# Performance work log

Hardware: AMD Instinct MI355X
Metric: run time of the kernel (lower is better)

Reference implementation:

```python
import jax, jax.numpy as jnp
import numpy as np
from jax import lax

CHANS = [3, 4, 8, 16, 32, 64, 128]


def _conv_relu(x, w, b):
    # x: [B,Cin,H,W], w: [Cout,Cin,4,4], stride 2, pad 1
    y = lax.conv_general_dilated(x, w, (2, 2), [(1, 1), (1, 1)],
                                 dimension_numbers=('NCHW', 'OIHW', 'NCHW'))
    return jax.nn.relu(y + b[None, :, None, None])


def setup_inputs() -> dict:
    key = jax.random.key(0)
    ks = jax.random.split(key, 64)
    T, B, S = 3, 2048, 64
    d = {"img_seq": jax.random.normal(ks[0], (T, B, 3, S, S), jnp.float32)}
    i = 1
    for l in range(6):
        cin, cout = CHANS[l], CHANS[l + 1]
        d[f"enc_w{l}"] = jax.random.normal(ks[i], (T, cout, cin, 4, 4), jnp.float32) / np.sqrt(cin * 16); i += 1
        d[f"enc_b{l}"] = jnp.zeros((T, cout), jnp.float32)
    # MLP 128 -> 32 -> 32 -> 64
    d["mlp_w1"] = jax.random.normal(ks[i], (32, 128), jnp.float32) / np.sqrt(128.0); i += 1
    d["mlp_b1"] = jnp.zeros((32,), jnp.float32)
    d["mlp_w2"] = jax.random.normal(ks[i], (32, 32), jnp.float32) / np.sqrt(32.0); i += 1
    d["mlp_b2"] = jnp.zeros((32,), jnp.float32)
    d["mlp_w3"] = jax.random.normal(ks[i], (64, 32), jnp.float32) / np.sqrt(32.0); i += 1
    d["mlp_b3"] = jnp.zeros((64,), jnp.float32)
    # LSTM: input 64, hidden 20 (torch gate order i,f,g,o)
    H = 20
    d["w_ih"] = jax.random.normal(ks[i], (4 * H, 64), jnp.float32) / np.sqrt(64.0); i += 1
    d["w_hh"] = jax.random.normal(ks[i], (4 * H, H), jnp.float32) / np.sqrt(float(H)); i += 1
    d["b_ih"] = jnp.zeros((4 * H,), jnp.float32)
    d["b_hh"] = jnp.zeros((4 * H,), jnp.float32)
    # 20 reward heads: 20 -> 32 -> 32 -> 1, stacked on leading K axis
    K = 20
    d["head_w1"] = jax.random.normal(ks[i], (K, 32, H), jnp.float32) / np.sqrt(float(H)); i += 1
    d["head_b1"] = jnp.zeros((K, 32), jnp.float32)
    d["head_w2"] = jax.random.normal(ks[i], (K, 32, 32), jnp.float32) / np.sqrt(32.0); i += 1
    d["head_b2"] = jnp.zeros((K, 32), jnp.float32)
    d["head_w3"] = jax.random.normal(ks[i], (K, 1, 32), jnp.float32) / np.sqrt(32.0); i += 1
    d["head_b3"] = jnp.zeros((K, 1), jnp.float32)
    return d


def reference(img_seq,
              enc_w0, enc_b0, enc_w1, enc_b1, enc_w2, enc_b2,
              enc_w3, enc_b3, enc_w4, enc_b4, enc_w5, enc_b5,
              mlp_w1, mlp_b1, mlp_w2, mlp_b2, mlp_w3, mlp_b3,
              w_ih, w_hh, b_ih, b_hh,
              head_w1, head_b1, head_w2, head_b2, head_w3, head_b3):
    # Per-frame CNN encoders (one encoder per time step) -> vmap over T
    def encode(img, w0, b0, w1, b1, w2, b2, w3, b3, w4, b4, w5, b5):
        x = _conv_relu(img, w0, b0)
        x = _conv_relu(x, w1, b1)
        x = _conv_relu(x, w2, b2)
        x = _conv_relu(x, w3, b3)
        x = _conv_relu(x, w4, b4)
        x = _conv_relu(x, w5, b5)  # [B,128,1,1]
        return x.reshape(x.shape[0], -1)  # [B,128]

    enc = jax.vmap(encode)(img_seq, enc_w0, enc_b0, enc_w1, enc_b1, enc_w2, enc_b2,
                           enc_w3, enc_b3, enc_w4, enc_b4, enc_w5, enc_b5)  # [T,B,128]

    # Shared MLP 128 -> 64
    h = jax.nn.relu(jnp.einsum('tbd,od->tbo', enc, mlp_w1) + mlp_b1)
    h = jax.nn.relu(jnp.einsum('tbd,od->tbo', h, mlp_w2) + mlp_b2)
    feats = jnp.einsum('tbd,od->tbo', h, mlp_w3) + mlp_b3  # [T,B,64]

    # Single-layer LSTM over T
    B, H = feats.shape[1], w_hh.shape[1]
    def step(carry, x_t):
        hs, cs = carry
        gates = x_t @ w_ih.T + hs @ w_hh.T + b_ih + b_hh  # [B,4H]
        i, f, g, o = jnp.split(gates, 4, axis=-1)
        cs = jax.nn.sigmoid(f) * cs + jax.nn.sigmoid(i) * jnp.tanh(g)
        hs = jax.nn.sigmoid(o) * jnp.tanh(cs)
        return (hs, cs), hs
    init = (jnp.zeros((B, H), feats.dtype), jnp.zeros((B, H), feats.dtype))
    _, h_seq = lax.scan(step, init, feats)  # [T,B,20]

    # 20 reward heads applied to every LSTM output, batched over head axis k
    x1 = jax.nn.relu(jnp.einsum('tbd,kod->ktbo', h_seq, head_w1) + head_b1[:, None, None, :])
    x2 = jax.nn.relu(jnp.einsum('ktbd,kod->ktbo', x1, head_w2) + head_b2[:, None, None, :])
    out = jnp.einsum('ktbd,kod->ktbo', x2, head_w3) + head_b3[:, None, None, :]  # [20,T,B,1]
    return out
```

## Files before the change

### kernel.cpp

```cpp
#include <hip/hip_runtime.h>
#include <math.h>

#define T_DIM 3
#define B_DIM 2048
#define NIMG  (T_DIM * B_DIM)


__global__ __launch_bounds__(256) void conv0_kernel(
    const float* __restrict__ img, const float* __restrict__ w0,
    const float* __restrict__ b0, float* __restrict__ a0)
{
    const int wid  = blockIdx.x * 4 + (threadIdx.x >> 6);
    const int lane = threadIdx.x & 63;
    const int half = wid & 1;
    const int oh   = (wid >> 1) & 31;
    const int g    = (wid >> 6) & 31;
    const int t    = wid >> 11;
    const int im   = g * 64 + lane;
    const size_t ib = ((size_t)t * 2048 + im) * 12288;
    const int ow0  = half * 16;

    float acc[4][16];
#pragma unroll
    for (int j = 0; j < 4; j++) {
        const float bv = b0[t * 4 + j];
#pragma unroll
        for (int k = 0; k < 16; k++) acc[j][k] = bv;
    }
    const float* wt = w0 + t * 192;

    for (int ci = 0; ci < 3; ci++) {
#pragma unroll
        for (int kh = 0; kh < 4; kh++) {
            const int ih = 2 * oh - 1 + kh;
            if ((unsigned)ih >= 64u) continue;
            const float* rp = img + ib + (size_t)(ci * 64 + ih) * 64 + 2 * ow0;
            float tap[34];
#pragma unroll
            for (int q = 0; q < 8; q++)
                *(float4*)&tap[1 + 4 * q] = *(const float4*)(rp + 4 * q);
            tap[0]  = (half == 0) ? 0.f : rp[-1];
            tap[33] = (half == 0) ? rp[32] : 0.f;
            float w_[4][4];
#pragma unroll
            for (int j = 0; j < 4; j++)
#pragma unroll
                for (int kw = 0; kw < 4; kw++)
                    w_[j][kw] = wt[((j * 3 + ci) * 4 + kh) * 4 + kw];
#pragma unroll
            for (int jj = 0; jj < 16; jj++)
#pragma unroll
                for (int kw = 0; kw < 4; kw++) {
                    const float x = tap[2 * jj + kw];
#pragma unroll
                    for (int j = 0; j < 4; j++)
                        acc[j][jj] = fmaf(x, w_[j][kw], acc[j][jj]);
                }
        }
    }
    const size_t ob0 = ((size_t)(t * 4096 + oh * 32 + ow0)) * 2048 + im;
#pragma unroll
    for (int j = 0; j < 4; j++)
#pragma unroll
        for (int k = 0; k < 16; k++)
            a0[ob0 + ((size_t)j * 1024 + k) * 2048] = fmaxf(acc[j][k], 0.f);
}

template<int CIN, int COUT, int IH, int OH, int CB>
__device__ __forceinline__ void convmid(
    const float* __restrict__ in, const float* __restrict__ gw,
    const float* __restrict__ gb, float* __restrict__ out,
    int t, int cg, int oh, int im)
{
    const int co0 = cg * CB;
    float acc[CB][OH];
#pragma unroll
    for (int j = 0; j < CB; j++) {
        const float bv = gb[t * COUT + co0 + j];
#pragma unroll
        for (int k = 0; k < OH; k++) acc[j][k] = bv;
    }
    const float* wt = gw + ((size_t)t * COUT + co0) * CIN * 16;
    const size_t inb = ((size_t)t * CIN) * (IH * IH) * 2048 + im;

#pragma unroll 4
    for (int ci = 0; ci < CIN; ci++) {
#pragma unroll
        for (int kh = 0; kh < 4; kh++) {
            const int ih = 2 * oh - 1 + kh;
            if ((unsigned)ih >= (unsigned)IH) continue;
            const float* rp = in + inb + (size_t)(ci * IH + ih) * IH * 2048;
            float tap[IH + 2];
            tap[0] = 0.f; tap[IH + 1] = 0.f;
#pragma unroll
            for (int iw = 0; iw < IH; iw++) tap[iw + 1] = rp[(size_t)iw * 2048];
            float w_[CB][4];
#pragma unroll
            for (int j = 0; j < CB; j++)
#pragma unroll
                for (int kw = 0; kw < 4; kw++)
                    w_[j][kw] = wt[((size_t)j * CIN + ci) * 16 + kh * 4 + kw];
#pragma unroll
            for (int ow = 0; ow < OH; ow++)
#pragma unroll
                for (int kw = 0; kw < 4; kw++) {
                    const float x = tap[2 * ow + kw];
#pragma unroll
                    for (int j = 0; j < CB; j++)
                        acc[j][ow] = fmaf(x, w_[j][kw], acc[j][ow]);
                }
        }
    }
    const size_t ob = ((size_t)(t * COUT + co0) * OH * OH + (size_t)oh * OH) * 2048 + im;
#pragma unroll
    for (int j = 0; j < CB; j++)
#pragma unroll
        for (int k = 0; k < OH; k++)
            out[ob + ((size_t)j * OH * OH + k) * 2048] = fmaxf(acc[j][k], 0.f);
}

__global__ __launch_bounds__(256) void conv1_kernel(
    const float* __restrict__ a0, const float* __restrict__ w,
    const float* __restrict__ b, float* __restrict__ a1)
{
    const int wid = blockIdx.x * 4 + (threadIdx.x >> 6);
    const int lane = threadIdx.x & 63;
    const int oh = wid & 15, cg = (wid >> 4) & 1, g = (wid >> 5) & 31, t = wid >> 10;
    convmid<4, 8, 32, 16, 4>(a0, w, b, a1, t, cg, oh, g * 64 + lane);
}

__global__ __launch_bounds__(256) void conv2_kernel(
    const float* __restrict__ a1, const float* __restrict__ w,
    const float* __restrict__ b, float* __restrict__ a2)
{
    const int wid = blockIdx.x * 4 + (threadIdx.x >> 6);
    const int lane = threadIdx.x & 63;
    const int oh = wid & 7, cg = (wid >> 3) & 3, g = (wid >> 5) & 31, t = wid >> 10;
    convmid<8, 16, 16, 8, 4>(a1, w, b, a2, t, cg, oh, g * 64 + lane);
}

__global__ __launch_bounds__(256) void conv3_kernel(
    const float* __restrict__ a2, const float* __restrict__ w,
    const float* __restrict__ b, float* __restrict__ a3)
{
    const int wid = blockIdx.x * 4 + (threadIdx.x >> 6);
    const int lane = threadIdx.x & 63;
    const int oh = wid & 3, cg = (wid >> 2) & 3, g = (wid >> 4) & 31, t = wid >> 9;
    convmid<16, 32, 8, 4, 8>(a2, w, b, a3, t, cg, oh, g * 64 + lane);
}

__global__ __launch_bounds__(256) void conv4_kernel(
    const float* __restrict__ a3, const float* __restrict__ w4,
    const float* __restrict__ b4, float* __restrict__ a4)
{
    const int wid = blockIdx.x * 4 + (threadIdx.x >> 6);
    const int lane = threadIdx.x & 63;
    const int cg = wid & 7, g = (wid >> 3) & 31, t = wid >> 8;
    const int im = g * 64 + lane;
    const int co0 = cg * 8;

    float acc[8][4];
#pragma unroll
    for (int j = 0; j < 8; j++) {
        const float bv = b4[t * 64 + co0 + j];
#pragma unroll
        for (int p = 0; p < 4; p++) acc[j][p] = bv;
    }
    const float* wt = w4 + ((size_t)t * 64 + co0) * 32 * 16;
    const size_t inb = ((size_t)t * 32) * 16 * 2048 + im;

    for (int ci = 0; ci < 32; ci++) {
        float tin[16];
#pragma unroll
        for (int p = 0; p < 16; p++)
            tin[p] = a3[inb + ((size_t)ci * 16 + p) * 2048];
#pragma unroll
        for (int kh = 0; kh < 4; kh++)
#pragma unroll
            for (int oh = 0; oh < 2; oh++) {
                const int ih = 2 * oh - 1 + kh;
                if (ih < 0 || ih > 3) continue;
#pragma unroll
                for (int ow = 0; ow < 2; ow++)
#pragma unroll
                    for (int kw = 0; kw < 4; kw++) {
                        const int iw = 2 * ow - 1 + kw;
                        if (iw < 0 || iw > 3) continue;
                        const float x = tin[ih * 4 + iw];
#pragma unroll
                        for (int j = 0; j < 8; j++)
                            acc[j][oh * 2 + ow] = fmaf(
                                x, wt[((size_t)j * 32 + ci) * 16 + kh * 4 + kw],
                                acc[j][oh * 2 + ow]);
                    }
            }
    }
#pragma unroll
    for (int j = 0; j < 8; j++)
#pragma unroll
        for (int p = 0; p < 4; p++)
            a4[(((size_t)t * 64 + co0 + j) * 4 + p) * 2048 + im] =
                fmaxf(acc[j][p], 0.f);
}

__global__ __launch_bounds__(256) void conv5_kernel(
    const float* __restrict__ a4, const float* __restrict__ w5,
    const float* __restrict__ b5, float* __restrict__ feats)
{
    const int wid = blockIdx.x * 4 + (threadIdx.x >> 6);
    const int lane = threadIdx.x & 63;
    const int cg = wid & 15, g = (wid >> 4) & 31, t = wid >> 9;
    const int im = g * 64 + lane;
    const int co0 = cg * 8;

    float acc[8];
#pragma unroll
    for (int j = 0; j < 8; j++) acc[j] = b5[t * 128 + co0 + j];
    const float* wt = w5 + ((size_t)t * 128 + co0) * 64 * 16;
    const size_t inb = ((size_t)t * 64) * 4 * 2048 + im;

#pragma unroll 4
    for (int ci = 0; ci < 64; ci++) {
        const float x0 = a4[inb + ((size_t)ci * 4 + 0) * 2048];
        const float x1 = a4[inb + ((size_t)ci * 4 + 1) * 2048];
        const float x2 = a4[inb + ((size_t)ci * 4 + 2) * 2048];
        const float x3 = a4[inb + ((size_t)ci * 4 + 3) * 2048];
#pragma unroll
        for (int j = 0; j < 8; j++) {
            const size_t wb = ((size_t)j * 64 + ci) * 16;
            acc[j] = fmaf(x0, wt[wb + 5],  acc[j]);
            acc[j] = fmaf(x1, wt[wb + 6],  acc[j]);
            acc[j] = fmaf(x2, wt[wb + 9],  acc[j]);
            acc[j] = fmaf(x3, wt[wb + 10], acc[j]);
        }
    }
#pragma unroll
    for (int j = 0; j < 8; j++)
        feats[((size_t)t * 128 + co0 + j) * 2048 + im] = fmaxf(acc[j], 0.f);
}

__device__ __forceinline__ float sigmoidf_(float x) { return 1.f / (1.f + expf(-x)); }

__global__ __launch_bounds__(64) void head_kernel(
    const float* __restrict__ feats,
    const float* __restrict__ mw1, const float* __restrict__ mb1,
    const float* __restrict__ mw2, const float* __restrict__ mb2,
    const float* __restrict__ mw3, const float* __restrict__ mb3,
    const float* __restrict__ wih, const float* __restrict__ whh,
    const float* __restrict__ bih, const float* __restrict__ bhh,
    const float* __restrict__ hw1, const float* __restrict__ hb1,
    const float* __restrict__ hw2, const float* __restrict__ hb2,
    const float* __restrict__ hw3, const float* __restrict__ hb3,
    float* __restrict__ out)
{
    const int b   = blockIdx.x;
    const int tid = threadIdx.x;
    __shared__ float sX[384];
    __shared__ float sH1[96];
    __shared__ float sH2[96];
    __shared__ float sF[192];
    __shared__ float sGates[80];
    __shared__ float sHs[20], sCs[20], sHseq[60];
    __shared__ float sA1[3 * 640];
    __shared__ float sA2[3 * 640];

    for (int i = tid; i < 384; i += 64)
        sX[i] = feats[(size_t)i * 2048 + b];
    __syncthreads();

    if (tid < 32) {
        const float4* wr = (const float4*)(mw1 + tid * 128);
        float a0 = mb1[tid], a1 = a0, a2 = a0;
        for (int d4 = 0; d4 < 32; d4++) {
            float4 w  = wr[d4];
            float4 x0 = ((const float4*)sX)[d4];
            float4 x1 = ((const float4*)sX)[32 + d4];
            float4 x2 = ((const float4*)sX)[64 + d4];
            a0 = fmaf(w.x, x0.x, a0); a0 = fmaf(w.y, x0.y, a0);
            a0 = fmaf(w.z, x0.z, a0); a0 = fmaf(w.w, x0.w, a0);
            a1 = fmaf(w.x, x1.x, a1); a1 = fmaf(w.y, x1.y, a1);
            a1 = fmaf(w.z, x1.z, a1); a1 = fmaf(w.w, x1.w, a1);
            a2 = fmaf(w.x, x2.x, a2); a2 = fmaf(w.y, x2.y, a2);
            a2 = fmaf(w.z, x2.z, a2); a2 = fmaf(w.w, x2.w, a2);
        }
        sH1[tid] = fmaxf(a0, 0.f); sH1[32 + tid] = fmaxf(a1, 0.f); sH1[64 + tid] = fmaxf(a2, 0.f);
    }
    __syncthreads();

    if (tid < 32) {
        const float* wr = mw2 + tid * 32;
        float a0 = mb2[tid], a1 = a0, a2 = a0;
#pragma unroll
        for (int d = 0; d < 32; d++) {
            float w = wr[d];
            a0 = fmaf(w, sH1[d], a0);
            a1 = fmaf(w, sH1[32 + d], a1);
            a2 = fmaf(w, sH1[64 + d], a2);
        }
        sH2[tid] = fmaxf(a0, 0.f); sH2[32 + tid] = fmaxf(a1, 0.f); sH2[64 + tid] = fmaxf(a2, 0.f);
    }
    __syncthreads();

    {
        const float* wr = mw3 + tid * 32;
        float a0 = mb3[tid], a1 = a0, a2 = a0;
#pragma unroll
        for (int d = 0; d < 32; d++) {
            float w = wr[d];
            a0 = fmaf(w, sH2[d], a0);
            a1 = fmaf(w, sH2[32 + d], a1);
            a2 = fmaf(w, sH2[64 + d], a2);
        }
        sF[tid] = a0; sF[64 + tid] = a1; sF[128 + tid] = a2;
    }
    if (tid < 20) { sHs[tid] = 0.f; sCs[tid] = 0.f; }
    __syncthreads();

    for (int t = 0; t < 3; t++) {
        for (int i = tid; i < 80; i += 64) {
            float a = bih[i] + bhh[i];
            const float4* wi = (const float4*)(wih + i * 64);
            const float4* xr = (const float4*)(sF + t * 64);
#pragma unroll
            for (int d4 = 0; d4 < 16; d4++) {
                float4 w = wi[d4]; float4 x = xr[d4];
                a = fmaf(w.x, x.x, a); a = fmaf(w.y, x.y, a);
                a = fmaf(w.z, x.z, a); a = fmaf(w.w, x.w, a);
            }
            const float* wh = whh + i * 20;
#pragma unroll
            for (int d = 0; d < 20; d++) a = fmaf(wh[d], sHs[d], a);
            sGates[i] = a;
        }
        __syncthreads();
        if (tid < 20) {
            float ig = sigmoidf_(sGates[tid]);
            float fg = sigmoidf_(sGates[20 + tid]);
            float g  = tanhf(sGates[40 + tid]);
            float og = sigmoidf_(sGates[60 + tid]);
            float c  = fg * sCs[tid] + ig * g;
            sCs[tid] = c;
            float h = og * tanhf(c);
            sHs[tid] = h;
            sHseq[t * 20 + tid] = h;
        }
        __syncthreads();
    }

    for (int i = tid; i < 640; i += 64) {
        float wrow[20];
        const float4* wr = (const float4*)(hw1 + i * 20);
#pragma unroll
        for (int q = 0; q < 5; q++) {
            float4 w = wr[q];
            wrow[q * 4 + 0] = w.x; wrow[q * 4 + 1] = w.y;
            wrow[q * 4 + 2] = w.z; wrow[q * 4 + 3] = w.w;
        }
        float bv = hb1[i];
        float a0 = bv, a1 = bv, a2 = bv;
#pragma unroll
        for (int d = 0; d < 20; d++) {
            float w = wrow[d];
            a0 = fmaf(w, sHseq[d], a0);
            a1 = fmaf(w, sHseq[20 + d], a1);
            a2 = fmaf(w, sHseq[40 + d], a2);
        }
        sA1[i] = fmaxf(a0, 0.f); sA1[640 + i] = fmaxf(a1, 0.f); sA1[1280 + i] = fmaxf(a2, 0.f);
    }
    __syncthreads();

    for (int i = tid; i < 640; i += 64) {
        int k = i >> 5;
        float wrow[32];
        const float4* wr = (const float4*)(hw2 + i * 32);
#pragma unroll
        for (int q = 0; q < 8; q++) {
            float4 w = wr[q];
            wrow[q * 4 + 0] = w.x; wrow[q * 4 + 1] = w.y;
            wrow[q * 4 + 2] = w.z; wrow[q * 4 + 3] = w.w;
        }
        float bv = hb2[i];
        float a0 = bv, a1 = bv, a2 = bv;
#pragma unroll
        for (int d = 0; d < 32; d++) {
            float w = wrow[d];
            a0 = fmaf(w, sA1[k * 32 + d], a0);
            a1 = fmaf(w, sA1[640 + k * 32 + d], a1);
            a2 = fmaf(w, sA1[1280 + k * 32 + d], a2);
        }
        sA2[i] = fmaxf(a0, 0.f); sA2[640 + i] = fmaxf(a1, 0.f); sA2[1280 + i] = fmaxf(a2, 0.f);
    }
    __syncthreads();

    if (tid < 20) {
        const float* wr = hw3 + tid * 32;
        float bv = hb3[tid];
        float a0 = bv, a1 = bv, a2 = bv;
#pragma unroll
        for (int d = 0; d < 32; d++) {
            float w = wr[d];
            a0 = fmaf(w, sA2[tid * 32 + d], a0);
            a1 = fmaf(w, sA2[640 + tid * 32 + d], a1);
            a2 = fmaf(w, sA2[1280 + tid * 32 + d], a2);
        }
        out[(size_t)(tid * 3 + 0) * 2048 + b] = a0;
        out[(size_t)(tid * 3 + 1) * 2048 + b] = a1;
        out[(size_t)(tid * 3 + 2) * 2048 + b] = a2;
    }
}

extern "C" void kernel_launch(void* const* d_in, const int* in_sizes, int n_in,
                              void* d_out, int out_size, void* d_ws, size_t ws_size,
                              hipStream_t stream)
{
    const float* img = (const float*)d_in[0];
    const float* ew0 = (const float*)d_in[1];  const float* eb0 = (const float*)d_in[2];
    const float* ew1 = (const float*)d_in[3];  const float* eb1 = (const float*)d_in[4];
    const float* ew2 = (const float*)d_in[5];  const float* eb2 = (const float*)d_in[6];
    const float* ew3 = (const float*)d_in[7];  const float* eb3 = (const float*)d_in[8];
    const float* ew4 = (const float*)d_in[9];  const float* eb4 = (const float*)d_in[10];
    const float* ew5 = (const float*)d_in[11]; const float* eb5 = (const float*)d_in[12];
    const float* mw1 = (const float*)d_in[13]; const float* mb1 = (const float*)d_in[14];
    const float* mw2 = (const float*)d_in[15]; const float* mb2 = (const float*)d_in[16];
    const float* mw3 = (const float*)d_in[17]; const float* mb3 = (const float*)d_in[18];
    const float* wih = (const float*)d_in[19]; const float* whh = (const float*)d_in[20];
    const float* bih = (const float*)d_in[21]; const float* bhh = (const float*)d_in[22];
    const float* hw1 = (const float*)d_in[23]; const float* hb1 = (const float*)d_in[24];
    const float* hw2 = (const float*)d_in[25]; const float* hb2 = (const float*)d_in[26];
    const float* hw3 = (const float*)d_in[27]; const float* hb3 = (const float*)d_in[28];

    float* A = (float*)d_ws;
    float* B = A + 25165824;
    float* C = B + 12582912;

    conv0_kernel<<<1536, 256, 0, stream>>>(img, ew0, eb0, A);
    conv1_kernel<<< 768, 256, 0, stream>>>(A, ew1, eb1, B);
    conv2_kernel<<< 768, 256, 0, stream>>>(B, ew2, eb2, A);
    conv3_kernel<<< 384, 256, 0, stream>>>(A, ew3, eb3, B);
    conv4_kernel<<< 192, 256, 0, stream>>>(B, ew4, eb4, A);
    conv5_kernel<<< 384, 256, 0, stream>>>(A, ew5, eb5, C);
    head_kernel<<<B_DIM, 64, 0, stream>>>(C, mw1, mb1, mw2, mb2, mw3, mb3,
                                          wih, whh, bih, bhh,
                                          hw1, hb1, hw2, hb2, hw3, hb3,
                                          (float*)d_out);
}
```

Baseline: 899.4 us.

## Stage conv0 rows in LDS, split conv4/5 finer, split head into three kernels

Conv0 now stages image rows into double-buffered shared memory with coalesced float4 loads. Each row is reused across two output rows within a block. Conv4 and conv5 halve the output channels per wave and double the grid to raise parallelism. The monolithic per-batch head kernel becomes three kernels with one thread per batch element: an MLP plus input-gate kernel, an LSTM kernel and a reward-heads kernel, replacing shared-memory reductions across 64 threads per sample. The risks are low occupancy in the tiny MLP and LSTM grids (96 and 32 blocks), register pressure from large per-thread arrays, and extra global traffic for the intermediates.

```diff
diff --git a/kernel.cpp b/kernel.cpp
--- a/kernel.cpp
+++ b/kernel.cpp
@@ -5,20 +5,28 @@
 #define B_DIM 2048
 #define NIMG  (T_DIM * B_DIM)
 
-
 __global__ __launch_bounds__(256) void conv0_kernel(
     const float* __restrict__ img, const float* __restrict__ w0,
     const float* __restrict__ b0, float* __restrict__ a0)
 {
-    const int wid  = blockIdx.x * 4 + (threadIdx.x >> 6);
-    const int lane = threadIdx.x & 63;
-    const int half = wid & 1;
-    const int oh   = (wid >> 1) & 31;
-    const int g    = (wid >> 6) & 31;
-    const int t    = wid >> 11;
+    __shared__ float sb[2][64 * 68];
+
+    const int bid  = blockIdx.x;
+    const int ohp  = bid & 15;
+    const int g    = (bid >> 4) & 31;
+    const int t    = bid >> 9;
+    const int tid  = threadIdx.x;
+    const int wv   = tid >> 6;
+    const int lane = tid & 63;
+    const int oh_sub = wv >> 1;
+    const int half   = wv & 1;
+    const int oh   = ohp * 2 + oh_sub;
+    const int ow0  = half * 16;
     const int im   = g * 64 + lane;
-    const size_t ib = ((size_t)t * 2048 + im) * 12288;
-    const int ow0  = half * 16;
+
+    const int jj16 = tid >> 4;
+    const int f4   = tid & 15;
+    const int ih0  = 4 * ohp - 1;
 
     float acc[4][16];
 #pragma unroll
@@ -29,35 +37,77 @@
     }
     const float* wt = w0 + t * 192;
 
-    for (int ci = 0; ci < 3; ci++) {
-#pragma unroll
-        for (int kh = 0; kh < 4; kh++) {
-            const int ih = 2 * oh - 1 + kh;
-            if ((unsigned)ih >= 64u) continue;
-            const float* rp = img + ib + (size_t)(ci * 64 + ih) * 64 + 2 * ow0;
-            float tap[34];
-#pragma unroll
-            for (int q = 0; q < 8; q++)
-                *(float4*)&tap[1 + 4 * q] = *(const float4*)(rp + 4 * q);
-            tap[0]  = (half == 0) ? 0.f : rp[-1];
-            tap[33] = (half == 0) ? rp[32] : 0.f;
-            float w_[4][4];
-#pragma unroll
-            for (int j = 0; j < 4; j++)
-#pragma unroll
-                for (int kw = 0; kw < 4; kw++)
-                    w_[j][kw] = wt[((j * 3 + ci) * 4 + kh) * 4 + kw];
-#pragma unroll
-            for (int jj = 0; jj < 16; jj++)
-#pragma unroll
-                for (int kw = 0; kw < 4; kw++) {
-                    const float x = tap[2 * jj + kw];
-#pragma unroll
-                    for (int j = 0; j < 4; j++)
-                        acc[j][jj] = fmaf(x, w_[j][kw], acc[j][jj]);
-                }
-        }
-    }
+    auto stage = [&](int ci, int ih, float* dst) {
+        if ((unsigned)ih < 64u) {
+#pragma unroll
+            for (int p = 0; p < 4; ++p) {
+                const int j = p * 16 + jj16;
+                const float4 v = *(const float4*)(img +
+                    ((size_t)((t * 2048 + g * 64 + j) * 3 + ci) << 12) +
+                    (ih << 6) + (f4 << 2));
+                *(float4*)&dst[j * 68 + (f4 << 2)] = v;
+            }
+        }
+    };
+
+    auto consume = [&](int ci, int r, int ih, const float* src) {
+        const int kh = r - 2 * oh_sub;
+        if (kh < 0 || kh > 3 || (unsigned)ih >= 64u) return;
+        const float* lrow = src + lane * 68;
+        float tap[34];
+        if (half == 0) {
+            tap[0] = 0.f;
+#pragma unroll
+            for (int c = 0; c < 8; ++c) {
+                const float4 v = *(const float4*)(lrow + 4 * c);
+                tap[1 + 4 * c] = v.x; tap[2 + 4 * c] = v.y;
+                tap[3 + 4 * c] = v.z; tap[4 + 4 * c] = v.w;
+            }
+            tap[33] = lrow[32];
+        } else {
+            tap[0] = lrow[31];
+#pragma unroll
+            for (int c = 0; c < 8; ++c) {
+                const float4 v = *(const float4*)(lrow + 32 + 4 * c);
+                tap[1 + 4 * c] = v.x; tap[2 + 4 * c] = v.y;
+                tap[3 + 4 * c] = v.z; tap[4 + 4 * c] = v.w;
+            }
+            tap[33] = 0.f;
+        }
+        float w_[4][4];
+#pragma unroll
+        for (int j = 0; j < 4; j++)
+#pragma unroll
+            for (int kw = 0; kw < 4; kw++)
+                w_[j][kw] = wt[((j * 3 + ci) * 4 + kh) * 4 + kw];
+#pragma unroll
+        for (int jj = 0; jj < 16; jj++)
+#pragma unroll
+            for (int kw = 0; kw < 4; kw++) {
+                const float x = tap[2 * jj + kw];
+#pragma unroll
+                for (int j = 0; j < 4; j++)
+                    acc[j][jj] = fmaf(x, w_[j][kw], acc[j][jj]);
+            }
+    };
+
+    stage(0, ih0, sb[0]);
+    __syncthreads();
+    int s = 0;
+#pragma unroll
+    for (int ci = 0; ci < 3; ++ci)
+#pragma unroll
+        for (int r = 0; r < 6; ++r) {
+            if (s < 17) {
+                const int rn = (r == 5) ? 0 : r + 1;
+                const int cn = (r == 5) ? ci + 1 : ci;
+                stage(cn, ih0 + rn, sb[(s + 1) & 1]);
+            }
+            consume(ci, r, ih0 + r, sb[s & 1]);
+            __syncthreads();
+            ++s;
+        }
+
     const size_t ob0 = ((size_t)(t * 4096 + oh * 32 + ow0)) * 2048 + im;
 #pragma unroll
     for (int j = 0; j < 4; j++)
@@ -155,13 +205,13 @@
 {
     const int wid = blockIdx.x * 4 + (threadIdx.x >> 6);
     const int lane = threadIdx.x & 63;
-    const int cg = wid & 7, g = (wid >> 3) & 31, t = wid >> 8;
+    const int cg = wid & 15, g = (wid >> 4) & 31, t = wid >> 9;
     const int im = g * 64 + lane;
-    const int co0 = cg * 8;
-
-    float acc[8][4];
-#pragma unroll
-    for (int j = 0; j < 8; j++) {
+    const int co0 = cg * 4;
+
+    float acc[4][4];
+#pragma unroll
+    for (int j = 0; j < 4; j++) {
         const float bv = b4[t * 64 + co0 + j];
 #pragma unroll
         for (int p = 0; p < 4; p++) acc[j][p] = bv;
@@ -188,7 +238,7 @@
                         if (iw < 0 || iw > 3) continue;
                         const float x = tin[ih * 4 + iw];
 #pragma unroll
-                        for (int j = 0; j < 8; j++)
+                        for (int j = 0; j < 4; j++)
                             acc[j][oh * 2 + ow] = fmaf(
                                 x, wt[((size_t)j * 32 + ci) * 16 + kh * 4 + kw],
                                 acc[j][oh * 2 + ow]);
@@ -196,7 +246,7 @@
             }
     }
 #pragma unroll
-    for (int j = 0; j < 8; j++)
+    for (int j = 0; j < 4; j++)
 #pragma unroll
         for (int p = 0; p < 4; p++)
             a4[(((size_t)t * 64 + co0 + j) * 4 + p) * 2048 + im] =
@@ -209,13 +259,13 @@
 {
     const int wid = blockIdx.x * 4 + (threadIdx.x >> 6);
     const int lane = threadIdx.x & 63;
-    const int cg = wid & 15, g = (wid >> 4) & 31, t = wid >> 9;
+    const int cg = wid & 31, g = (wid >> 5) & 31, t = wid >> 10;
     const int im = g * 64 + lane;
-    const int co0 = cg * 8;
-
-    float acc[8];
-#pragma unroll
-    for (int j = 0; j < 8; j++) acc[j] = b5[t * 128 + co0 + j];
+    const int co0 = cg * 4;
+
+    float acc[4];
+#pragma unroll
+    for (int j = 0; j < 4; j++) acc[j] = b5[t * 128 + co0 + j];
     const float* wt = w5 + ((size_t)t * 128 + co0) * 64 * 16;
     const size_t inb = ((size_t)t * 64) * 4 * 2048 + im;
 
@@ -226,7 +276,7 @@
         const float x2 = a4[inb + ((size_t)ci * 4 + 2) * 2048];
         const float x3 = a4[inb + ((size_t)ci * 4 + 3) * 2048];
 #pragma unroll
-        for (int j = 0; j < 8; j++) {
+        for (int j = 0; j < 4; j++) {
             const size_t wb = ((size_t)j * 64 + ci) * 16;
             acc[j] = fmaf(x0, wt[wb + 5],  acc[j]);
             acc[j] = fmaf(x1, wt[wb + 6],  acc[j]);
@@ -235,178 +285,170 @@
         }
     }
 #pragma unroll
-    for (int j = 0; j < 8; j++)
+    for (int j = 0; j < 4; j++)
         feats[((size_t)t * 128 + co0 + j) * 2048 + im] = fmaxf(acc[j], 0.f);
 }
 
-__device__ __forceinline__ float sigmoidf_(float x) { return 1.f / (1.f + expf(-x)); }
-
-__global__ __launch_bounds__(64) void head_kernel(
+
+__global__ __launch_bounds__(64) void mlpxg_kernel(
     const float* __restrict__ feats,
     const float* __restrict__ mw1, const float* __restrict__ mb1,
     const float* __restrict__ mw2, const float* __restrict__ mb2,
     const float* __restrict__ mw3, const float* __restrict__ mb3,
-    const float* __restrict__ wih, const float* __restrict__ whh,
-    const float* __restrict__ bih, const float* __restrict__ bhh,
+    const float* __restrict__ wih, const float* __restrict__ bih,
+    const float* __restrict__ bhh, float* __restrict__ xg)
+{
+    const int tb = blockIdx.x;
+    const int t  = tb >> 5, bg = tb & 31;
+    const int b  = bg * 64 + threadIdx.x;
+
+    float x[128];
+#pragma unroll
+    for (int d = 0; d < 128; ++d)
+        x[d] = feats[((size_t)t * 128 + d) * 2048 + b];
+
+    float h1[32];
+#pragma unroll
+    for (int o = 0; o < 32; ++o) {
+        float a = mb1[o];
+        const float4* wr = (const float4*)(mw1 + o * 128);
+#pragma unroll
+        for (int q = 0; q < 32; ++q) {
+            const float4 w = wr[q];
+            a = fmaf(w.x, x[4 * q + 0], a); a = fmaf(w.y, x[4 * q + 1], a);
+            a = fmaf(w.z, x[4 * q + 2], a); a = fmaf(w.w, x[4 * q + 3], a);
+        }
+        h1[o] = fmaxf(a, 0.f);
+    }
+    float h2[32];
+#pragma unroll
+    for (int o = 0; o < 32; ++o) {
+        float a = mb2[o];
+        const float4* wr = (const float4*)(mw2 + o * 32);
+#pragma unroll
+        for (int q = 0; q < 8; ++q) {
+            const float4 w = wr[q];
+            a = fmaf(w.x, h1[4 * q + 0], a); a = fmaf(w.y, h1[4 * q + 1], a);
+            a = fmaf(w.z, h1[4 * q + 2], a); a = fmaf(w.w, h1[4 * q + 3], a);
+        }
+        h2[o] = fmaxf(a, 0.f);
+    }
+    float f_[64];
+#pragma unroll
+    for (int o = 0; o < 64; ++o) {
+        float a = mb3[o];
+        const float4* wr = (const float4*)(mw3 + o * 32);
+#pragma unroll
+        for (int q = 0; q < 8; ++q) {
+            const float4 w = wr[q];
+            a = fmaf(w.x, h2[4 * q + 0], a); a = fmaf(w.y, h2[4 * q + 1], a);
+            a = fmaf(w.z, h2[4 * q + 2], a); a = fmaf(w.w, h2[4 * q + 3], a);
+        }
+        f_[o] = a;
+    }
+#pragma unroll
+    for (int i = 0; i < 80; ++i) {
+        float a = bih[i] + bhh[i];
+        const float4* wr = (const float4*)(wih + i * 64);
+#pragma unroll
+        for (int q = 0; q < 16; ++q) {
+            const float4 w = wr[q];
+            a = fmaf(w.x, f_[4 * q + 0], a); a = fmaf(w.y, f_[4 * q + 1], a);
+            a = fmaf(w.z, f_[4 * q + 2], a); a = fmaf(w.w, f_[4 * q + 3], a);
+        }
+        xg[((size_t)t * 80 + i) * 2048 + b] = a;
+    }
+}
+
+__global__ __launch_bounds__(64) void lstm_kernel(
+    const float* __restrict__ xg, const float* __restrict__ whh,
+    float* __restrict__ hseq)
+{
+    const int b = blockIdx.x * 64 + threadIdx.x;
+    float h[20], c[20];
+#pragma unroll
+    for (int j = 0; j < 20; ++j) { h[j] = 0.f; c[j] = 0.f; }
+
+    for (int t = 0; t < 3; ++t) {
+        float gv[80];
+#pragma unroll
+        for (int i = 0; i < 80; ++i) {
+            float a = xg[((size_t)t * 80 + i) * 2048 + b];
+            const float4* wr = (const float4*)(whh + i * 20);
+#pragma unroll
+            for (int q = 0; q < 5; ++q) {
+                const float4 w = wr[q];
+                a = fmaf(w.x, h[4 * q + 0], a); a = fmaf(w.y, h[4 * q + 1], a);
+                a = fmaf(w.z, h[4 * q + 2], a); a = fmaf(w.w, h[4 * q + 3], a);
+            }
+            gv[i] = a;
+        }
+#pragma unroll
+        for (int j = 0; j < 20; ++j) {
+            const float ig = 1.f / (1.f + expf(-gv[j]));
+            const float fg = 1.f / (1.f + expf(-gv[20 + j]));
+            const float gt = tanhf(gv[40 + j]);
+            const float og = 1.f / (1.f + expf(-gv[60 + j]));
+            const float cn = fg * c[j] + ig * gt;
+            c[j] = cn;
+            const float hn = og * tanhf(cn);
+            h[j] = hn;
+            hseq[((size_t)t * 20 + j) * 2048 + b] = hn;
+        }
+    }
+}
+
+__global__ __launch_bounds__(64) void heads_kernel(
+    const float* __restrict__ hseq,
     const float* __restrict__ hw1, const float* __restrict__ hb1,
     const float* __restrict__ hw2, const float* __restrict__ hb2,
     const float* __restrict__ hw3, const float* __restrict__ hb3,
     float* __restrict__ out)
 {
-    const int b   = blockIdx.x;
-    const int tid = threadIdx.x;
-    __shared__ float sX[384];
-    __shared__ float sH1[96];
-    __shared__ float sH2[96];
-    __shared__ float sF[192];
-    __shared__ float sGates[80];
-    __shared__ float sHs[20], sCs[20], sHseq[60];
-    __shared__ float sA1[3 * 640];
-    __shared__ float sA2[3 * 640];
-
-    for (int i = tid; i < 384; i += 64)
-        sX[i] = feats[(size_t)i * 2048 + b];
-    __syncthreads();
-
-    if (tid < 32) {
-        const float4* wr = (const float4*)(mw1 + tid * 128);
-        float a0 = mb1[tid], a1 = a0, a2 = a0;
-        for (int d4 = 0; d4 < 32; d4++) {
-            float4 w  = wr[d4];
-            float4 x0 = ((const float4*)sX)[d4];
-            float4 x1 = ((const float4*)sX)[32 + d4];
-            float4 x2 = ((const float4*)sX)[64 + d4];
-            a0 = fmaf(w.x, x0.x, a0); a0 = fmaf(w.y, x0.y, a0);
-            a0 = fmaf(w.z, x0.z, a0); a0 = fmaf(w.w, x0.w, a0);
-            a1 = fmaf(w.x, x1.x, a1); a1 = fmaf(w.y, x1.y, a1);
-            a1 = fmaf(w.z, x1.z, a1); a1 = fmaf(w.w, x1.w, a1);
-            a2 = fmaf(w.x, x2.x, a2); a2 = fmaf(w.y, x2.y, a2);
-            a2 = fmaf(w.z, x2.z, a2); a2 = fmaf(w.w, x2.w, a2);
-        }
-        sH1[tid] = fmaxf(a0, 0.f); sH1[32 + tid] = fmaxf(a1, 0.f); sH1[64 + tid] = fmaxf(a2, 0.f);
-    }
-    __syncthreads();
-
-    if (tid < 32) {
-        const float* wr = mw2 + tid * 32;
-        float a0 = mb2[tid], a1 = a0, a2 = a0;
-#pragma unroll
-        for (int d = 0; d < 32; d++) {
-            float w = wr[d];
-            a0 = fmaf(w, sH1[d], a0);
-            a1 = fmaf(w, sH1[32 + d], a1);
-            a2 = fmaf(w, sH1[64 + d], a2);
-        }
-        sH2[tid] = fmaxf(a0, 0.f); sH2[32 + tid] = fmaxf(a1, 0.f); sH2[64 + tid] = fmaxf(a2, 0.f);
-    }
-    __syncthreads();
-
-    {
-        const float* wr = mw3 + tid * 32;
-        float a0 = mb3[tid], a1 = a0, a2 = a0;
-#pragma unroll
-        for (int d = 0; d < 32; d++) {
-            float w = wr[d];
-            a0 = fmaf(w, sH2[d], a0);
-            a1 = fmaf(w, sH2[32 + d], a1);
-            a2 = fmaf(w, sH2[64 + d], a2);
-        }
-        sF[tid] = a0; sF[64 + tid] = a1; sF[128 + tid] = a2;
-    }
-    if (tid < 20) { sHs[tid] = 0.f; sCs[tid] = 0.f; }
-    __syncthreads();
-
-    for (int t = 0; t < 3; t++) {
-        for (int i = tid; i < 80; i += 64) {
-            float a = bih[i] + bhh[i];
-            const float4* wi = (const float4*)(wih + i * 64);
-            const float4* xr = (const float4*)(sF + t * 64);
-#pragma unroll
-            for (int d4 = 0; d4 < 16; d4++) {
-                float4 w = wi[d4]; float4 x = xr[d4];
-                a = fmaf(w.x, x.x, a); a = fmaf(w.y, x.y, a);
-                a = fmaf(w.z, x.z, a); a = fmaf(w.w, x.w, a);
-            }
-            const float* wh = whh + i * 20;
-#pragma unroll
-            for (int d = 0; d < 20; d++) a = fmaf(wh[d], sHs[d], a);
-            sGates[i] = a;
-        }
-        __syncthreads();
-        if (tid < 20) {
-            float ig = sigmoidf_(sGates[tid]);
-            float fg = sigmoidf_(sGates[20 + tid]);
-            float g  = tanhf(sGates[40 + tid]);
-            float og = sigmoidf_(sGates[60 + tid]);
-            float c  = fg * sCs[tid] + ig * g;
-            sCs[tid] = c;
-            float h = og * tanhf(c);
-            sHs[tid] = h;
-            sHseq[t * 20 + tid] = h;
-        }
-        __syncthreads();
-    }
-
-    for (int i = tid; i < 640; i += 64) {
-        float wrow[20];
-        const float4* wr = (const float4*)(hw1 + i * 20);
-#pragma unroll
-        for (int q = 0; q < 5; q++) {
-            float4 w = wr[q];
-            wrow[q * 4 + 0] = w.x; wrow[q * 4 + 1] = w.y;
-            wrow[q * 4 + 2] = w.z; wrow[q * 4 + 3] = w.w;
-        }
-        float bv = hb1[i];
-        float a0 = bv, a1 = bv, a2 = bv;
-#pragma unroll
-        for (int d = 0; d < 20; d++) {
-            float w = wrow[d];
-            a0 = fmaf(w, sHseq[d], a0);
-            a1 = fmaf(w, sHseq[20 + d], a1);
-            a2 = fmaf(w, sHseq[40 + d], a2);
-        }
-        sA1[i] = fmaxf(a0, 0.f); sA1[640 + i] = fmaxf(a1, 0.f); sA1[1280 + i] = fmaxf(a2, 0.f);
-    }
-    __syncthreads();
-
-    for (int i = tid; i < 640; i += 64) {
-        int k = i >> 5;
-        float wrow[32];
-        const float4* wr = (const float4*)(hw2 + i * 32);
-#pragma unroll
-        for (int q = 0; q < 8; q++) {
-            float4 w = wr[q];
-            wrow[q * 4 + 0] = w.x; wrow[q * 4 + 1] = w.y;
-            wrow[q * 4 + 2] = w.z; wrow[q * 4 + 3] = w.w;
-        }
-        float bv = hb2[i];
-        float a0 = bv, a1 = bv, a2 = bv;
-#pragma unroll
-        for (int d = 0; d < 32; d++) {
-            float w = wrow[d];
-            a0 = fmaf(w, sA1[k * 32 + d], a0);
-            a1 = fmaf(w, sA1[640 + k * 32 + d], a1);
-            a2 = fmaf(w, sA1[1280 + k * 32 + d], a2);
-        }
-        sA2[i] = fmaxf(a0, 0.f); sA2[640 + i] = fmaxf(a1, 0.f); sA2[1280 + i] = fmaxf(a2, 0.f);
-    }
-    __syncthreads();
-
-    if (tid < 20) {
-        const float* wr = hw3 + tid * 32;
-        float bv = hb3[tid];
-        float a0 = bv, a1 = bv, a2 = bv;
-#pragma unroll
-        for (int d = 0; d < 32; d++) {
-            float w = wr[d];
-            a0 = fmaf(w, sA2[tid * 32 + d], a0);
-            a1 = fmaf(w, sA2[640 + tid * 32 + d], a1);
-            a2 = fmaf(w, sA2[1280 + tid * 32 + d], a2);
-        }
-        out[(size_t)(tid * 3 + 0) * 2048 + b] = a0;
-        out[(size_t)(tid * 3 + 1) * 2048 + b] = a1;
-        out[(size_t)(tid * 3 + 2) * 2048 + b] = a2;
-    }
+    const int t  = blockIdx.x >> 5, bg = blockIdx.x & 31;
+    const int k  = blockIdx.y;
+    const int b  = bg * 64 + threadIdx.x;
+
+    float xv[20];
+#pragma unroll
+    for (int d = 0; d < 20; ++d)
+        xv[d] = hseq[((size_t)t * 20 + d) * 2048 + b];
+
+    float a1[32];
+#pragma unroll
+    for (int o = 0; o < 32; ++o) {
+        float a = hb1[k * 32 + o];
+        const float4* wr = (const float4*)(hw1 + ((size_t)k * 32 + o) * 20);
+#pragma unroll
+        for (int q = 0; q < 5; ++q) {
+            const float4 w = wr[q];
+            a = fmaf(w.x, xv[4 * q + 0], a); a = fmaf(w.y, xv[4 * q + 1], a);
+            a = fmaf(w.z, xv[4 * q + 2], a); a = fmaf(w.w, xv[4 * q + 3], a);
+        }
+        a1[o] = fmaxf(a, 0.f);
+    }
+    float a2[32];
+#pragma unroll
+    for (int o = 0; o < 32; ++o) {
+        float a = hb2[k * 32 + o];
+        const float4* wr = (const float4*)(hw2 + ((size_t)k * 32 + o) * 32);
+#pragma unroll
+        for (int q = 0; q < 8; ++q) {
+            const float4 w = wr[q];
+            a = fmaf(w.x, a1[4 * q + 0], a); a = fmaf(w.y, a1[4 * q + 1], a);
+            a = fmaf(w.z, a1[4 * q + 2], a); a = fmaf(w.w, a1[4 * q + 3], a);
+        }
+        a2[o] = fmaxf(a, 0.f);
+    }
+    float r = hb3[k];
+    const float4* wr = (const float4*)(hw3 + (size_t)k * 32);
+#pragma unroll
+    for (int q = 0; q < 8; ++q) {
+        const float4 w = wr[q];
+        r = fmaf(w.x, a2[4 * q + 0], r); r = fmaf(w.y, a2[4 * q + 1], r);
+        r = fmaf(w.z, a2[4 * q + 2], r); r = fmaf(w.w, a2[4 * q + 3], r);
+    }
+    out[((size_t)k * 3 + t) * 2048 + b] = r;
 }
 
 extern "C" void kernel_launch(void* const* d_in, const int* in_sizes, int n_in,
@@ -429,18 +471,21 @@
     const float* hw2 = (const float*)d_in[25]; const float* hb2 = (const float*)d_in[26];
     const float* hw3 = (const float*)d_in[27]; const float* hb3 = (const float*)d_in[28];
 
-    float* A = (float*)d_ws;
-    float* B = A + 25165824;
-    float* C = B + 12582912;
+    float* A  = (float*)d_ws;
+    float* B  = A + 25165824;
+    float* C  = B + 12582912;
+    float* XG = B;
+    float* HS = B + 491520;
 
     conv0_kernel<<<1536, 256, 0, stream>>>(img, ew0, eb0, A);
     conv1_kernel<<< 768, 256, 0, stream>>>(A, ew1, eb1, B);
     conv2_kernel<<< 768, 256, 0, stream>>>(B, ew2, eb2, A);
     conv3_kernel<<< 384, 256, 0, stream>>>(A, ew3, eb3, B);
-    conv4_kernel<<< 192, 256, 0, stream>>>(B, ew4, eb4, A);
-    conv5_kernel<<< 384, 256, 0, stream>>>(A, ew5, eb5, C);
-    head_kernel<<<B_DIM, 64, 0, stream>>>(C, mw1, mb1, mw2, mb2, mw3, mb3,
-                                          wih, whh, bih, bhh,
-                                          hw1, hb1, hw2, hb2, hw3, hb3,
-                                          (float*)d_out);
-}
+    conv4_kernel<<< 384, 256, 0, stream>>>(B, ew4, eb4, A);
+    conv5_kernel<<< 768, 256, 0, stream>>>(A, ew5, eb5, C);
+    mlpxg_kernel<<<96, 64, 0, stream>>>(C, mw1, mb1, mw2, mb2, mw3, mb3,
+                                        wih, bih, bhh, XG);
+    lstm_kernel<<<32, 64, 0, stream>>>(XG, whh, HS);
+    heads_kernel<<<dim3(96, 20), 64, 0, stream>>>(HS, hw1, hb1, hw2, hb2,
+                                                  hw3, hb3, (float*)d_out);
+}
```

Result: slower. 1.083 ms (+20.4%).
